# Kernel optimization log

Measured on AMD Instinct MI355X. Metric: run time of the kernel, lower is better.

The kernel has to match this reference:

```python
import jax, jax.numpy as jnp
import numpy as np

BS = 128          # block size for fp8 block-scaled quantization
FP8_MAX = 448.0   # max normal value of float8_e4m3fn


def _weight_quant(w):
    """Quantize weight [O, I] with per-(128x128)-block scales, DeepSeek-V3 style.
    Returns (w_q stored as fp32 holding fp8-representable values, scale [O/BS, I/BS])."""
    O, I = w.shape
    wb = w.reshape(O // BS, BS, I // BS, BS)
    amax = jnp.max(jnp.abs(wb), axis=(1, 3))
    scale = jnp.where(amax == 0, 1.0, amax / FP8_MAX)
    q = (wb / scale[:, None, :, None]).astype(jnp.float8_e4m3fn).astype(jnp.float32)
    return q.reshape(O, I), scale


def _act_qdq(x):
    """act_quant + dequant: per-128-block (last dim) fp8 quantization of activations."""
    T, D = x.shape
    xb = x.reshape(T, D // BS, BS)
    amax = jnp.max(jnp.abs(xb), axis=-1, keepdims=True)
    scale = jnp.where(amax == 0, 1.0, amax / FP8_MAX)
    q = (xb / scale).astype(jnp.float8_e4m3fn).astype(jnp.float32)
    return (q * scale).reshape(T, D)


def _dequant_w(wq, ws):
    O, I = wq.shape
    return (wq.reshape(O // BS, BS, I // BS, BS) * ws[:, None, :, None]).reshape(O, I)


def _linear_fp8(x, wq, ws):
    # fp8_gemm with per-block scales == dequantized GEMM in fp32 accumulate
    return _act_qdq(x) @ _dequant_w(wq, ws).T


def setup_inputs() -> dict:
    T, DIM, INTER = 2048, 4096, 11008
    key = jax.random.key(0)
    kx, k1, k2, k3 = jax.random.split(key, 4)
    x = jax.random.normal(kx, (T, DIM), dtype=jnp.float32)
    w1 = jax.random.normal(k1, (INTER, DIM), dtype=jnp.float32) * 0.02
    w2 = jax.random.normal(k2, (DIM, INTER), dtype=jnp.float32) * 0.02
    w3 = jax.random.normal(k3, (INTER, DIM), dtype=jnp.float32) * 0.02
    w1_q, w1_s = _weight_quant(w1)
    w2_q, w2_s = _weight_quant(w2)
    w3_q, w3_s = _weight_quant(w3)
    return {"x": x, "w1_q": w1_q, "w1_s": w1_s, "w2_q": w2_q, "w2_s": w2_s,
            "w3_q": w3_q, "w3_s": w3_s}


def reference(x, w1_q, w1_s, w2_q, w2_s, w3_q, w3_s):
    # SwiGLU: w2( silu(w1(x)) * w3(x) ), each linear is fp8 block-scaled GEMM
    h = jax.nn.silu(_linear_fp8(x, w1_q, w1_s)) * _linear_fp8(x, w3_q, w3_s)
    return _linear_fp8(h, w2_q, w2_s)
```

## Files before the change

kernel.cpp:

```cpp
#include <hip/hip_runtime.h>
#include <hip/hip_fp8.h>

#define T_DIM 2048
#define D_DIM 4096
#define I_DIM 11008

typedef int v8i __attribute__((ext_vector_type(8)));
typedef float v4f __attribute__((ext_vector_type(4)));

__device__ inline unsigned char to_fp8(float f) {
  return (unsigned char)__hip_cvt_float_to_fp8(f, __HIP_SATFINITE, __HIP_E4M3);
}

__device__ inline void async_copy16(const void* g, void* l) {
  __builtin_amdgcn_global_load_lds((const __attribute__((address_space(1))) void*)g,
                                   (__attribute__((address_space(3))) void*)l, 16, 0, 0);
}

__global__ void quant_x_kernel(const float* __restrict__ X, unsigned char* __restrict__ Q,
                               float* __restrict__ St, const int T, const int D) {
  const int wave = (blockIdx.x << 2) + (threadIdx.x >> 6);
  const int lane = threadIdx.x & 63;
  const int nb = D >> 7;
  const int t = wave / nb;
  const int kb = wave - t * nb;
  const size_t base = (size_t)t * D + ((size_t)kb << 7);
  const float2 v = ((const float2*)(X + base))[lane];
  float a = fmaxf(fabsf(v.x), fabsf(v.y));
#pragma unroll
  for (int off = 32; off > 0; off >>= 1) a = fmaxf(a, __shfl_xor(a, off));
  const float scale = (a == 0.f) ? 1.f : (a / 448.f);
  unsigned short pk = (unsigned short)to_fp8(v.x / scale) |
                      ((unsigned short)to_fp8(v.y / scale) << 8);
  ((unsigned short*)(Q + base))[lane] = pk;
  if (lane == 0) St[(size_t)kb * T + t] = scale;
}

__global__ void silu_mul_quant_kernel(const float* __restrict__ H1, const float* __restrict__ H3,
                                      unsigned char* __restrict__ Q, float* __restrict__ St,
                                      const int T, const int D) {
  const int wave = (blockIdx.x << 2) + (threadIdx.x >> 6);
  const int lane = threadIdx.x & 63;
  const int nb = D >> 7;
  const int t = wave / nb;
  const int kb = wave - t * nb;
  const size_t base = (size_t)t * D + ((size_t)kb << 7);
  const float2 v1 = ((const float2*)(H1 + base))[lane];
  const float2 v3 = ((const float2*)(H3 + base))[lane];
  const float hx = (v1.x / (1.f + expf(-v1.x))) * v3.x;
  const float hy = (v1.y / (1.f + expf(-v1.y))) * v3.y;
  float a = fmaxf(fabsf(hx), fabsf(hy));
#pragma unroll
  for (int off = 32; off > 0; off >>= 1) a = fmaxf(a, __shfl_xor(a, off));
  const float scale = (a == 0.f) ? 1.f : (a / 448.f);
  unsigned short pk = (unsigned short)to_fp8(hx / scale) |
                      ((unsigned short)to_fp8(hy / scale) << 8);
  ((unsigned short*)(Q + base))[lane] = pk;
  if (lane == 0) St[(size_t)kb * T + t] = scale;
}

__global__ void convert_fp8_kernel(const float4* __restrict__ W, unsigned int* __restrict__ Q,
                                   const int n4) {
  const int i = blockIdx.x * 256 + threadIdx.x;
  if (i >= n4) return;
  const float4 f = W[i];
  Q[i] = (unsigned int)to_fp8(f.x) | ((unsigned int)to_fp8(f.y) << 8) |
         ((unsigned int)to_fp8(f.z) << 16) | ((unsigned int)to_fp8(f.w) << 24);
}

__global__ __launch_bounds__(256, 2) void gemm_fp8_bs(
    const unsigned char* __restrict__ A, const float* __restrict__ sAt,
    const unsigned char* __restrict__ B, const float* __restrict__ sB,
    float* __restrict__ C, const int M, const int N, const int K) {
  __shared__ unsigned char As[128 * 128];
  __shared__ unsigned char Bs[128 * 128];

  const int tid = threadIdx.x;
  const int lane = tid & 63;
  const int w = tid >> 6;
  const int wm = (w >> 1) << 6;
  const int wn = (w & 1) << 6;
  const int row16 = lane & 15;
  const int quad = lane >> 4;
  const int m0 = blockIdx.x << 7;
  const int n0 = blockIdx.y << 7;
  const int nkb = K >> 7;

  const int srow = (w << 5) + (lane >> 3);
  const int scol = (lane & 7) << 4;
  const unsigned char* gA = A + (size_t)(m0 + srow) * K + scol;
  const unsigned char* gB = B + (size_t)(n0 + srow) * K + scol;
  unsigned char* lA = &As[w << 12];
  unsigned char* lB = &Bs[w << 12];

  v4f zero = {0.f, 0.f, 0.f, 0.f};
  v4f acc[4][4];
#pragma unroll
  for (int i = 0; i < 4; ++i)
#pragma unroll
    for (int j = 0; j < 4; ++j) acc[i][j] = zero;

  const float* sArow = sAt + m0 + wm + (quad << 2);
  const float* sBrow = sB + (size_t)(n0 >> 7) * nkb;

  for (int kb = 0; kb < nkb; ++kb) {
    __syncthreads();
    const size_t koff = (size_t)kb << 7;
#pragma unroll
    for (int t = 0; t < 4; ++t)
      async_copy16(gA + (size_t)(t * 8) * K + koff, lA + (t << 10));
#pragma unroll
    for (int t = 0; t < 4; ++t)
      async_copy16(gB + (size_t)(t * 8) * K + koff, lB + (t << 10));

    const float sb = sBrow[kb];
    float4 sa[4];
    const float4* sap = (const float4*)(sArow + (size_t)kb * M);
#pragma unroll
    for (int i = 0; i < 4; ++i) sa[i] = sap[i * 4];

    __syncthreads();

    v8i a[4], b[4];
#pragma unroll
    for (int i = 0; i < 4; ++i)
      a[i] = *(const v8i*)&As[((wm + (i << 4) + row16) << 7) + (quad << 5)];
#pragma unroll
    for (int j = 0; j < 4; ++j)
      b[j] = *(const v8i*)&Bs[((wn + (j << 4) + row16) << 7) + (quad << 5)];

#pragma unroll
    for (int i = 0; i < 4; ++i) {
      v4f cs;
      cs.x = sa[i].x * sb; cs.y = sa[i].y * sb;
      cs.z = sa[i].z * sb; cs.w = sa[i].w * sb;
#pragma unroll
      for (int j = 0; j < 4; ++j) {
        v4f p = __builtin_amdgcn_mfma_scale_f32_16x16x128_f8f6f4(
            a[i], b[j], zero, 0, 0, 0, 0x7f7f7f7f, 0, 0x7f7f7f7f);
        acc[i][j] += cs * p;
      }
    }
  }

#pragma unroll
  for (int i = 0; i < 4; ++i) {
    const size_t rbase = (size_t)(m0 + wm + (i << 4) + (quad << 2));
#pragma unroll
    for (int r = 0; r < 4; ++r) {
      float* crow = C + (rbase + r) * N + n0 + wn + row16;
#pragma unroll
      for (int j = 0; j < 4; ++j) crow[j << 4] = acc[i][j][r];
    }
  }
}

extern "C" void kernel_launch(void* const* d_in, const int* in_sizes, int n_in,
                              void* d_out, int out_size, void* d_ws, size_t ws_size,
                              hipStream_t stream) {
  const float* x   = (const float*)d_in[0];
  const float* w1q = (const float*)d_in[1];
  const float* w1s = (const float*)d_in[2];
  const float* w2q = (const float*)d_in[3];
  const float* w2s = (const float*)d_in[4];
  const float* w3q = (const float*)d_in[5];
  const float* w3s = (const float*)d_in[6];

  unsigned char* ws = (unsigned char*)d_ws;
  const size_t SZ_QX = (size_t)T_DIM * D_DIM;
  const size_t SZ_W  = (size_t)I_DIM * D_DIM;
  const size_t SZ_QH = (size_t)T_DIM * I_DIM;
  const size_t SZ_SX = (size_t)(D_DIM / 128) * T_DIM * 4;
  const size_t SZ_SH = (size_t)(I_DIM / 128) * T_DIM * 4;
  const size_t SZ_H  = (size_t)T_DIM * I_DIM * 4;

  unsigned char* qx   = ws;             ws += SZ_QX;
  unsigned char* w1q8 = ws;             ws += SZ_W;
  unsigned char* w3q8 = ws;             ws += SZ_W;
  unsigned char* w2q8 = ws;             ws += SZ_W;
  unsigned char* qh   = ws;             ws += SZ_QH;
  float* sxt = (float*)ws;              ws += SZ_SX;
  float* sht = (float*)ws;              ws += SZ_SH;
  float* h1  = (float*)ws;              ws += SZ_H;
  float* h3  = (float*)ws;              ws += SZ_H;

  quant_x_kernel<<<(T_DIM * (D_DIM / 128)) / 4, 256, 0, stream>>>(x, qx, sxt, T_DIM, D_DIM);

  const int n4w = (int)(SZ_W / 4);
  convert_fp8_kernel<<<(n4w + 255) / 256, 256, 0, stream>>>((const float4*)w1q, (unsigned int*)w1q8, n4w);
  convert_fp8_kernel<<<(n4w + 255) / 256, 256, 0, stream>>>((const float4*)w3q, (unsigned int*)w3q8, n4w);
  convert_fp8_kernel<<<(n4w + 255) / 256, 256, 0, stream>>>((const float4*)w2q, (unsigned int*)w2q8, n4w);

  dim3 g13(T_DIM / 128, I_DIM / 128);
  gemm_fp8_bs<<<g13, 256, 0, stream>>>(qx, sxt, w1q8, w1s, h1, T_DIM, I_DIM, D_DIM);
  gemm_fp8_bs<<<g13, 256, 0, stream>>>(qx, sxt, w3q8, w3s, h3, T_DIM, I_DIM, D_DIM);

  silu_mul_quant_kernel<<<(T_DIM * (I_DIM / 128)) / 4, 256, 0, stream>>>(h1, h3, qh, sht, T_DIM, I_DIM);

  dim3 g2(T_DIM / 128, D_DIM / 128);
  gemm_fp8_bs<<<g2, 256, 0, stream>>>(qh, sht, w2q8, w2s, (float*)d_out, T_DIM, D_DIM, I_DIM);

  (void)in_sizes; (void)n_in; (void)out_size; (void)ws_size;
}
```

Before: 1.022 ms.

## Double-buffer LDS tiles in fp8 GEMM and use packed fp8 conversion

The GEMM now keeps two LDS buffers for A and B tiles and prefetches the next K-block (and its scales) while computing on the current one, with one barrier per step instead of two. K is made a compile-time template parameter and the loop is unrolled by two. The quantization kernels switch to the hardware packed fp8 convert builtin and a fast exp. LDS use doubles per block and the loop assumes an even number of K-blocks.

```diff
diff --git a/kernel.cpp b/kernel.cpp
--- a/kernel.cpp
+++ b/kernel.cpp
@@ -7,10 +7,6 @@
 
 typedef int v8i __attribute__((ext_vector_type(8)));
 typedef float v4f __attribute__((ext_vector_type(4)));
-
-__device__ inline unsigned char to_fp8(float f) {
-  return (unsigned char)__hip_cvt_float_to_fp8(f, __HIP_SATFINITE, __HIP_E4M3);
-}
 
 __device__ inline void async_copy16(const void* g, void* l) {
   __builtin_amdgcn_global_load_lds((const __attribute__((address_space(1))) void*)g,
@@ -30,8 +26,7 @@
 #pragma unroll
   for (int off = 32; off > 0; off >>= 1) a = fmaxf(a, __shfl_xor(a, off));
   const float scale = (a == 0.f) ? 1.f : (a / 448.f);
-  unsigned short pk = (unsigned short)to_fp8(v.x / scale) |
-                      ((unsigned short)to_fp8(v.y / scale) << 8);
+  unsigned short pk = (unsigned short)__builtin_amdgcn_cvt_pk_fp8_f32(v.x / scale, v.y / scale, 0, false);
   ((unsigned short*)(Q + base))[lane] = pk;
   if (lane == 0) St[(size_t)kb * T + t] = scale;
 }
@@ -47,14 +42,13 @@
   const size_t base = (size_t)t * D + ((size_t)kb << 7);
   const float2 v1 = ((const float2*)(H1 + base))[lane];
   const float2 v3 = ((const float2*)(H3 + base))[lane];
-  const float hx = (v1.x / (1.f + expf(-v1.x))) * v3.x;
-  const float hy = (v1.y / (1.f + expf(-v1.y))) * v3.y;
+  const float hx = (v1.x / (1.f + __expf(-v1.x))) * v3.x;
+  const float hy = (v1.y / (1.f + __expf(-v1.y))) * v3.y;
   float a = fmaxf(fabsf(hx), fabsf(hy));
 #pragma unroll
   for (int off = 32; off > 0; off >>= 1) a = fmaxf(a, __shfl_xor(a, off));
   const float scale = (a == 0.f) ? 1.f : (a / 448.f);
-  unsigned short pk = (unsigned short)to_fp8(hx / scale) |
-                      ((unsigned short)to_fp8(hy / scale) << 8);
+  unsigned short pk = (unsigned short)__builtin_amdgcn_cvt_pk_fp8_f32(hx / scale, hy / scale, 0, false);
   ((unsigned short*)(Q + base))[lane] = pk;
   if (lane == 0) St[(size_t)kb * T + t] = scale;
 }
@@ -64,16 +58,65 @@
   const int i = blockIdx.x * 256 + threadIdx.x;
   if (i >= n4) return;
   const float4 f = W[i];
-  Q[i] = (unsigned int)to_fp8(f.x) | ((unsigned int)to_fp8(f.y) << 8) |
-         ((unsigned int)to_fp8(f.z) << 16) | ((unsigned int)to_fp8(f.w) << 24);
-}
-
+  int r = __builtin_amdgcn_cvt_pk_fp8_f32(f.x, f.y, 0, false);
+  r = __builtin_amdgcn_cvt_pk_fp8_f32(f.z, f.w, r, true);
+  Q[i] = (unsigned int)r;
+}
+
+__device__ inline void stage_tiles(const unsigned char* gA, const unsigned char* gB,
+                                   unsigned char* lA, unsigned char* lB,
+                                   size_t koff, const int K) {
+#pragma unroll
+  for (int t = 0; t < 4; ++t)
+    async_copy16(gA + (size_t)(t * 8) * K + koff, lA + (t << 10));
+#pragma unroll
+  for (int t = 0; t < 4; ++t)
+    async_copy16(gB + (size_t)(t * 8) * K + koff, lB + (t << 10));
+}
+
+__device__ inline void load_scales(const float* __restrict__ sArow, const float* __restrict__ sBrow,
+                                   int kb, int M, float4 sa[4], float& sb) {
+  const float4* sap = (const float4*)(sArow + (size_t)kb * M);
+#pragma unroll
+  for (int i = 0; i < 4; ++i) sa[i] = sap[i * 4];
+  sb = sBrow[kb];
+}
+
+__device__ inline void compute_step(const unsigned char* __restrict__ Asb,
+                                    const unsigned char* __restrict__ Bsb,
+                                    int wm, int wn, int row16, int quad,
+                                    const float4 sa[4], float sb, v4f acc[4][4]) {
+  v4f zero = {0.f, 0.f, 0.f, 0.f};
+  v8i a[4], b[4];
+#pragma unroll
+  for (int i = 0; i < 4; ++i)
+    a[i] = *(const v8i*)&Asb[((wm + (i << 4) + row16) << 7) + (quad << 5)];
+#pragma unroll
+  for (int j = 0; j < 4; ++j)
+    b[j] = *(const v8i*)&Bsb[((wn + (j << 4) + row16) << 7) + (quad << 5)];
+
+#pragma unroll
+  for (int i = 0; i < 4; ++i) {
+    v4f cs;
+    cs.x = sa[i].x * sb; cs.y = sa[i].y * sb;
+    cs.z = sa[i].z * sb; cs.w = sa[i].w * sb;
+#pragma unroll
+    for (int j = 0; j < 4; ++j) {
+      v4f p = __builtin_amdgcn_mfma_scale_f32_16x16x128_f8f6f4(
+          a[i], b[j], zero, 0, 0, 0, 0x7f7f7f7f, 0, 0x7f7f7f7f);
+      acc[i][j] += cs * p;
+    }
+  }
+}
+
+template <int NKB>
 __global__ __launch_bounds__(256, 2) void gemm_fp8_bs(
     const unsigned char* __restrict__ A, const float* __restrict__ sAt,
     const unsigned char* __restrict__ B, const float* __restrict__ sB,
-    float* __restrict__ C, const int M, const int N, const int K) {
-  __shared__ unsigned char As[128 * 128];
-  __shared__ unsigned char Bs[128 * 128];
+    float* __restrict__ C, const int M, const int N) {
+  const int K = NKB << 7;
+  __shared__ unsigned char As[2][128 * 128];
+  __shared__ unsigned char Bs[2][128 * 128];
 
   const int tid = threadIdx.x;
   const int lane = tid & 63;
@@ -84,63 +127,43 @@
   const int quad = lane >> 4;
   const int m0 = blockIdx.x << 7;
   const int n0 = blockIdx.y << 7;
-  const int nkb = K >> 7;
 
   const int srow = (w << 5) + (lane >> 3);
   const int scol = (lane & 7) << 4;
   const unsigned char* gA = A + (size_t)(m0 + srow) * K + scol;
   const unsigned char* gB = B + (size_t)(n0 + srow) * K + scol;
-  unsigned char* lA = &As[w << 12];
-  unsigned char* lB = &Bs[w << 12];
-
-  v4f zero = {0.f, 0.f, 0.f, 0.f};
+  unsigned char* lA0 = &As[0][w << 12];
+  unsigned char* lB0 = &Bs[0][w << 12];
+  unsigned char* lA1 = &As[1][w << 12];
+  unsigned char* lB1 = &Bs[1][w << 12];
+
   v4f acc[4][4];
 #pragma unroll
   for (int i = 0; i < 4; ++i)
 #pragma unroll
-    for (int j = 0; j < 4; ++j) acc[i][j] = zero;
+    for (int j = 0; j < 4; ++j) acc[i][j] = (v4f){0.f, 0.f, 0.f, 0.f};
 
   const float* sArow = sAt + m0 + wm + (quad << 2);
-  const float* sBrow = sB + (size_t)(n0 >> 7) * nkb;
-
-  for (int kb = 0; kb < nkb; ++kb) {
+  const float* sBrow = sB + (size_t)(n0 >> 7) * NKB;
+
+  float4 sa_c[4], sa_n[4];
+  float sb_c, sb_n;
+
+  load_scales(sArow, sBrow, 0, M, sa_c, sb_c);
+  stage_tiles(gA, gB, lA0, lB0, 0, K);
+  __syncthreads();
+
+  for (int kb = 0; kb < NKB; kb += 2) {
+    stage_tiles(gA, gB, lA1, lB1, (size_t)(kb + 1) << 7, K);
+    load_scales(sArow, sBrow, kb + 1, M, sa_n, sb_n);
+    compute_step(&As[0][0], &Bs[0][0], wm, wn, row16, quad, sa_c, sb_c, acc);
     __syncthreads();
-    const size_t koff = (size_t)kb << 7;
-#pragma unroll
-    for (int t = 0; t < 4; ++t)
-      async_copy16(gA + (size_t)(t * 8) * K + koff, lA + (t << 10));
-#pragma unroll
-    for (int t = 0; t < 4; ++t)
-      async_copy16(gB + (size_t)(t * 8) * K + koff, lB + (t << 10));
-
-    const float sb = sBrow[kb];
-    float4 sa[4];
-    const float4* sap = (const float4*)(sArow + (size_t)kb * M);
-#pragma unroll
-    for (int i = 0; i < 4; ++i) sa[i] = sap[i * 4];
-
+
+    const int kb2 = (kb + 2 < NKB) ? kb + 2 : 0;
+    if (kb + 2 < NKB) stage_tiles(gA, gB, lA0, lB0, (size_t)(kb + 2) << 7, K);
+    load_scales(sArow, sBrow, kb2, M, sa_c, sb_c);
+    compute_step(&As[1][0], &Bs[1][0], wm, wn, row16, quad, sa_n, sb_n, acc);
     __syncthreads();
-
-    v8i a[4], b[4];
-#pragma unroll
-    for (int i = 0; i < 4; ++i)
-      a[i] = *(const v8i*)&As[((wm + (i << 4) + row16) << 7) + (quad << 5)];
-#pragma unroll
-    for (int j = 0; j < 4; ++j)
-      b[j] = *(const v8i*)&Bs[((wn + (j << 4) + row16) << 7) + (quad << 5)];
-
-#pragma unroll
-    for (int i = 0; i < 4; ++i) {
-      v4f cs;
-      cs.x = sa[i].x * sb; cs.y = sa[i].y * sb;
-      cs.z = sa[i].z * sb; cs.w = sa[i].w * sb;
-#pragma unroll
-      for (int j = 0; j < 4; ++j) {
-        v4f p = __builtin_amdgcn_mfma_scale_f32_16x16x128_f8f6f4(
-            a[i], b[j], zero, 0, 0, 0, 0x7f7f7f7f, 0, 0x7f7f7f7f);
-        acc[i][j] += cs * p;
-      }
-    }
   }
 
 #pragma unroll
@@ -192,13 +215,13 @@
   convert_fp8_kernel<<<(n4w + 255) / 256, 256, 0, stream>>>((const float4*)w2q, (unsigned int*)w2q8, n4w);
 
   dim3 g13(T_DIM / 128, I_DIM / 128);
-  gemm_fp8_bs<<<g13, 256, 0, stream>>>(qx, sxt, w1q8, w1s, h1, T_DIM, I_DIM, D_DIM);
-  gemm_fp8_bs<<<g13, 256, 0, stream>>>(qx, sxt, w3q8, w3s, h3, T_DIM, I_DIM, D_DIM);
+  gemm_fp8_bs<D_DIM / 128><<<g13, 256, 0, stream>>>(qx, sxt, w1q8, w1s, h1, T_DIM, I_DIM);
+  gemm_fp8_bs<D_DIM / 128><<<g13, 256, 0, stream>>>(qx, sxt, w3q8, w3s, h3, T_DIM, I_DIM);
 
   silu_mul_quant_kernel<<<(T_DIM * (I_DIM / 128)) / 4, 256, 0, stream>>>(h1, h3, qh, sht, T_DIM, I_DIM);
 
   dim3 g2(T_DIM / 128, D_DIM / 128);
-  gemm_fp8_bs<<<g2, 256, 0, stream>>>(qh, sht, w2q8, w2s, (float*)d_out, T_DIM, D_DIM, I_DIM);
+  gemm_fp8_bs<I_DIM / 128><<<g2, 256, 0, stream>>>(qh, sht, w2q8, w2s, (float*)d_out, T_DIM, D_DIM);
 
   (void)in_sizes; (void)n_in; (void)out_size; (void)ws_size;
 }
```

After: 1.031 ms. Within noise of the previous version (+0.9%).
